# Performance work log

Measured on AMD Instinct MI355X. Metric: run time of the kernel, lower is better.

Reference implementation:

```python
import jax, jax.numpy as jnp
import numpy as np

B, NI, D, P, R = 32, 1024, 1024, 1000, 3  # batch, patches, d_model, pool_size, agg rounds


def setup_inputs() -> dict:
    key = jax.random.key(0)
    ks = jax.random.split(key, 12)
    w = lambda k, shape: jax.random.normal(k, shape, jnp.float32) * 0.02
    return {
        "att_feats": jax.random.normal(ks[0], (B, NI, D), jnp.float32),
        "fc_feats": jax.random.normal(ks[1], (B, D), jnp.float32),
        "pool": jax.random.normal(ks[2], (P, D), jnp.float32),
        "W_agg": w(ks[3], (R, D, D)),          # stacked agg projections (no bias)
        "Wq": w(ks[4], (D, D)), "bq": jnp.zeros((D,), jnp.float32),
        "Wk": w(ks[5], (D, D)), "bk": jnp.zeros((D,), jnp.float32),
        "Wv": w(ks[6], (D, D)), "bv": jnp.zeros((D,), jnp.float32),
        "Wc": w(ks[7], (D, D)), "bc": jnp.zeros((D,), jnp.float32),
        "Wg": w(ks[8], (2 * D,)), "bg": jnp.asarray(-1.0, jnp.float32),  # gate bias init -1
        "residual_scale": jnp.asarray(0.1, jnp.float32),
    }


def reference(att_feats, fc_feats, pool, W_agg, Wq, bq, Wk, bk, Wv, bv, Wc, bc, Wg, bg, residual_scale):
    d = att_feats.shape[-1]
    scale = 1.0 / jnp.sqrt(jnp.asarray(d, att_feats.dtype))
    v_hat = fc_feats  # fc dim == d_model path

    # Aggregate attention: R rounds over normality pool, averaged (Eq. 4-6)
    q_all = jnp.einsum('bd,rod->rbo', v_hat, W_agg)            # [R,B,D]
    scores = jnp.einsum('rbo,po->rbp', q_all, pool) * scale    # [R,B,P]
    weights = jax.nn.softmax(scores, axis=-1)
    v_agg = jnp.einsum('rbp,pd->bd', weights, pool) / R        # [B,D]

    # Differentiate attention (Eq. 7-10)
    q = v_hat @ Wq.T + bq
    k = v_agg @ Wk.T + bk
    v = v_agg @ Wv.T + bv
    sim = jnp.sum(q * k, axis=-1, keepdims=True) * scale       # [B,1]
    v_common = jax.nn.sigmoid(sim) * v
    v_diff = jax.nn.relu((v_hat - v_common) @ Wc.T + bc)       # [B,D] (dropout = identity, eval)

    # Gated residual; split gate weight to avoid materializing the concat
    Wg1, Wg2 = Wg[:d], Wg[d:]
    g = jax.nn.sigmoid(att_feats @ Wg1 + (v_diff @ Wg2)[:, None] + bg)  # [B,NI]
    return att_feats + residual_scale * g[..., None] * v_diff[:, None, :]
```

## Files before the change

kernel.cpp:

```cpp
#include <hip/hip_runtime.h>

#define D 1024
#define B 32
#define NI 1024
#define PP 1000
#define R 3
#define SPLITS 8
#define VS 8
#define BK 32
#define KT (D / SPLITS / BK)
#define PAD 34

typedef float f32x4_t __attribute__((ext_vector_type(4)));

__device__ __forceinline__ void nt_store4(float* p, float4 v) {
    f32x4_t x = {v.x, v.y, v.z, v.w};
    __builtin_nontemporal_store(x, (f32x4_t*)p);
}

__device__ __forceinline__ float wred(float x) {
    #pragma unroll
    for (int off = 32; off; off >>= 1) x += __shfl_xor(x, off, 64);
    return x;
}
__device__ __forceinline__ float wmax(float x) {
    #pragma unroll
    for (int off = 32; off; off >>= 1) x = fmaxf(x, __shfl_xor(x, off, 64));
    return x;
}

template<int NXS>
__device__ __forceinline__ void gemm_core(
        const float* __restrict__ A, int mbase, int Mrows,
        const float* __restrict__ Xb, int xrstride, size_t xss,
        int kc0, float acc[4][4]) {
    __shared__ float Ws[128][PAD];
    __shared__ float Xs[32][PAD];
    const int t = threadIdx.x;
    const int ty = t >> 3, tx = t & 7;
    const int m0 = 4 * ty, b0 = 4 * tx;
    const int lrow = t >> 3, lq = t & 7;

    #pragma unroll
    for (int i = 0; i < 4; ++i)
        #pragma unroll
        for (int j = 0; j < 4; ++j) acc[i][j] = 0.f;

    for (int kt = 0; kt < KT; ++kt) {
        const int kc = kc0 + kt * BK;
        #pragma unroll
        for (int rr = 0; rr < 4; ++rr) {
            const int row = lrow + 32 * rr;
            float4 v = make_float4(0.f, 0.f, 0.f, 0.f);
            if (mbase + row < Mrows)
                v = *(const float4*)(A + (size_t)(mbase + row) * D + kc + 4 * lq);
            *(float2*)&Ws[row][4 * lq]     = make_float2(v.x, v.y);
            *(float2*)&Ws[row][4 * lq + 2] = make_float2(v.z, v.w);
        }
        {
            const float* xp = Xb + (size_t)lrow * xrstride + kc + 4 * lq;
            float4 v = *(const float4*)xp;
            #pragma unroll
            for (int s = 1; s < NXS; ++s) {
                float4 w = *(const float4*)(xp + (size_t)s * xss);
                v.x += w.x; v.y += w.y; v.z += w.z; v.w += w.w;
            }
            *(float2*)&Xs[lrow][4 * lq]     = make_float2(v.x, v.y);
            *(float2*)&Xs[lrow][4 * lq + 2] = make_float2(v.z, v.w);
        }
        __syncthreads();
        #pragma unroll
        for (int kp = 0; kp < 16; ++kp) {
            float2 wv[4], xv[4];
            #pragma unroll
            for (int i = 0; i < 4; ++i) wv[i] = *(const float2*)&Ws[m0 + i][2 * kp];
            #pragma unroll
            for (int j = 0; j < 4; ++j) xv[j] = *(const float2*)&Xs[b0 + j][2 * kp];
            #pragma unroll
            for (int i = 0; i < 4; ++i)
                #pragma unroll
                for (int j = 0; j < 4; ++j) {
                    acc[i][j] += wv[i].x * xv[j].x;
                    acc[i][j] += wv[i].y * xv[j].y;
                }
        }
        __syncthreads();
    }
}

__global__ __launch_bounds__(256) void gemm_k1(const float* __restrict__ Wagg,
        const float* __restrict__ fc, float* __restrict__ Cp) {
    const int mb = blockIdx.x, s = blockIdx.y;
    const int mbase = mb * 128;
    float acc[4][4];
    gemm_core<1>(Wagg, mbase, R * D, fc, D, 0, s * 128, acc);
    const int t = threadIdx.x, ty = t >> 3, tx = t & 7;
    const int m = mbase + 4 * ty;
    #pragma unroll
    for (int j = 0; j < 4; ++j) {
        float* cp = Cp + ((size_t)(s * B) + 4 * tx + j) * (R * D) + m;
        *(float4*)cp = make_float4(acc[0][j], acc[1][j], acc[2][j], acc[3][j]);
    }
}

__global__ __launch_bounds__(256) void gemm_k2(const float* __restrict__ pool,
        const float* __restrict__ qallp, float* __restrict__ Cp) {
    const int mb = blockIdx.x, s = blockIdx.y, r = blockIdx.z;
    const int mbase = mb * 128;
    float acc[4][4];
    gemm_core<SPLITS>(pool, mbase, PP, qallp + r * D, R * D, (size_t)B * R * D,
                      s * 128, acc);
    const int t = threadIdx.x, ty = t >> 3, tx = t & 7;
    const int m = mbase + 4 * ty;
    if (m >= PP) return;
    #pragma unroll
    for (int j = 0; j < 4; ++j) {
        float* cp = Cp + ((size_t)((s * R + r) * B) + 4 * tx + j) * D + m;
        *(float4*)cp = make_float4(acc[0][j], acc[1][j], acc[2][j], acc[3][j]);
    }
}

__global__ __launch_bounds__(256) void gemm_k5q(const float* __restrict__ Wq,
        const float* __restrict__ fc, float* __restrict__ Cp) {
    const int mb = blockIdx.x, s = blockIdx.y;
    const int mbase = mb * 128;
    float acc[4][4];
    gemm_core<1>(Wq, mbase, D, fc, D, 0, s * 128, acc);
    const int t = threadIdx.x, ty = t >> 3, tx = t & 7;
    const int m = mbase + 4 * ty;
    #pragma unroll
    for (int j = 0; j < 4; ++j) {
        float* cp = Cp + ((size_t)((s * R + 0) * B) + 4 * tx + j) * D + m;
        *(float4*)cp = make_float4(acc[0][j], acc[1][j], acc[2][j], acc[3][j]);
    }
}

__global__ __launch_bounds__(256) void gemm_k5kv(const float* __restrict__ Wk,
        const float* __restrict__ Wv, const float* __restrict__ vaggp,
        float* __restrict__ Cp) {
    const int mb = blockIdx.x, s = blockIdx.y, z = blockIdx.z;
    const int mbase = mb * 128;
    const float* A = (z == 0) ? Wk : Wv;
    float acc[4][4];
    gemm_core<VS>(A, mbase, D, vaggp, D, (size_t)B * D, s * 128, acc);
    const int t = threadIdx.x, ty = t >> 3, tx = t & 7;
    const int m = mbase + 4 * ty;
    #pragma unroll
    for (int j = 0; j < 4; ++j) {
        float* cp = Cp + ((size_t)((s * R + z + 1) * B) + 4 * tx + j) * D + m;
        *(float4*)cp = make_float4(acc[0][j], acc[1][j], acc[2][j], acc[3][j]);
    }
}

__global__ __launch_bounds__(256) void gemm_k7(const float* __restrict__ Wc,
        const float* __restrict__ u, float* __restrict__ Cp) {
    const int mb = blockIdx.x, s = blockIdx.y;
    const int mbase = mb * 128;
    float acc[4][4];
    gemm_core<1>(Wc, mbase, D, u, D, 0, s * 128, acc);
    const int t = threadIdx.x, ty = t >> 3, tx = t & 7;
    const int m = mbase + 4 * ty;
    #pragma unroll
    for (int j = 0; j < 4; ++j) {
        float* cp = Cp + ((size_t)(s * B) + 4 * tx + j) * D + m;
        *(float4*)cp = make_float4(acc[0][j], acc[1][j], acc[2][j], acc[3][j]);
    }
}

__global__ __launch_bounds__(256) void k3_wbar(const float* __restrict__ scp,
        float* __restrict__ wbar) {
    const int b = blockIdx.x;
    const int t = threadIdx.x, w = t >> 6, lane = t & 63;
    __shared__ float red[8];
    float wb[4] = {0.f, 0.f, 0.f, 0.f};
    for (int r = 0; r < R; ++r) {
        float v[4];
        float mx = -1e30f;
        #pragma unroll
        for (int i = 0; i < 4; ++i) {
            const int p = t + 256 * i;
            float x = -1e30f;
            if (p < PP) {
                x = 0.f;
                #pragma unroll
                for (int s = 0; s < SPLITS; ++s)
                    x += scp[((size_t)((s * R + r) * B) + b) * D + p];
                x *= 0.03125f;
            }
            v[i] = x;
            mx = fmaxf(mx, x);
        }
        mx = wmax(mx);
        if (lane == 0) red[w] = mx;
        __syncthreads();
        mx = fmaxf(fmaxf(red[0], red[1]), fmaxf(red[2], red[3]));
        float e[4], sum = 0.f;
        #pragma unroll
        for (int i = 0; i < 4; ++i) {
            const int p = t + 256 * i;
            e[i] = (p < PP) ? __expf(v[i] - mx) : 0.f;
            sum += e[i];
        }
        sum = wred(sum);
        if (lane == 0) red[4 + w] = sum;
        __syncthreads();
        const float inv = 1.f / (red[4] + red[5] + red[6] + red[7]);
        #pragma unroll
        for (int i = 0; i < 4; ++i) wb[i] += e[i] * inv;
        __syncthreads();
    }
    #pragma unroll
    for (int i = 0; i < 4; ++i) {
        const int p = t + 256 * i;
        wbar[(size_t)b * 1024 + p] = wb[i] * (1.f / 3.f);
    }
}

__global__ __launch_bounds__(256) void k4_vagg(const float* __restrict__ wbar,
        const float* __restrict__ pool, float* __restrict__ vaggp) {
    const int db = blockIdx.x, ps = blockIdx.y;
    __shared__ float Ps[32][132];
    __shared__ float Wbt[32][36];
    const int t = threadIdx.x;
    const int ty = t >> 3, tx = t & 7;
    float acc[4][4];
    #pragma unroll
    for (int i = 0; i < 4; ++i)
        #pragma unroll
        for (int j = 0; j < 4; ++j) acc[i][j] = 0.f;

    for (int pt = 0; pt < 4; ++pt) {
        const int p0 = ps * 128 + pt * 32;
        {
            const int prow = t >> 5, qc = t & 31;
            #pragma unroll
            for (int rr = 0; rr < 4; ++rr) {
                const int pr = prow + 8 * rr;
                float4 v = make_float4(0.f, 0.f, 0.f, 0.f);
                if (p0 + pr < PP)
                    v = *(const float4*)(pool + (size_t)(p0 + pr) * D + db * 128 + 4 * qc);
                *(float4*)&Ps[pr][4 * qc] = v;
            }
        }
        {
            const int bb = t >> 3, q = t & 7;
            float4 v = *(const float4*)(wbar + (size_t)bb * 1024 + p0 + 4 * q);
            Wbt[4 * q + 0][bb] = v.x; Wbt[4 * q + 1][bb] = v.y;
            Wbt[4 * q + 2][bb] = v.z; Wbt[4 * q + 3][bb] = v.w;
        }
        __syncthreads();
        #pragma unroll
        for (int pg = 0; pg < 8; ++pg) {
            #pragma unroll
            for (int pp = 0; pp < 4; ++pp) {
                const int p = 4 * pg + pp;
                float4 xv = *(const float4*)&Ps[p][4 * ty];
                float4 wv = *(const float4*)&Wbt[p][4 * tx];
                const float xs[4] = {xv.x, xv.y, xv.z, xv.w};
                const float wsv[4] = {wv.x, wv.y, wv.z, wv.w};
                #pragma unroll
                for (int i = 0; i < 4; ++i)
                    #pragma unroll
                    for (int j = 0; j < 4; ++j)
                        acc[i][j] += xs[i] * wsv[j];
            }
        }
        __syncthreads();
    }
    const int dbase = db * 128 + 4 * ty;
    #pragma unroll
    for (int j = 0; j < 4; ++j) {
        float* op = vaggp + ((size_t)ps * B + 4 * tx + j) * D + dbase;
        *(float4*)op = make_float4(acc[0][j], acc[1][j], acc[2][j], acc[3][j]);
    }
}

__global__ __launch_bounds__(256) void k6_u(const float* __restrict__ qkvp,
        const float* __restrict__ bq, const float* __restrict__ bk,
        const float* __restrict__ bv, const float* __restrict__ vhat,
        float* __restrict__ u) {
    const int b = blockIdx.x;
    const int t = threadIdx.x, w = t >> 6, lane = t & 63;
    const int d = 4 * t;
    float4 qv = *(const float4*)(bq + d);
    float4 kv = *(const float4*)(bk + d);
    #pragma unroll
    for (int s = 0; s < SPLITS; ++s) {
        float4 a = *(const float4*)(qkvp + ((size_t)((s * R + 0) * B) + b) * D + d);
        float4 c = *(const float4*)(qkvp + ((size_t)((s * R + 1) * B) + b) * D + d);
        qv.x += a.x; qv.y += a.y; qv.z += a.z; qv.w += a.w;
        kv.x += c.x; kv.y += c.y; kv.z += c.z; kv.w += c.w;
    }
    float local = qv.x * kv.x + qv.y * kv.y + qv.z * kv.z + qv.w * kv.w;
    local = wred(local);
    __shared__ float red[4];
    if (lane == 0) red[w] = local;
    __syncthreads();
    const float sim = (red[0] + red[1] + red[2] + red[3]) * 0.03125f;
    const float sig = 1.f / (1.f + __expf(-sim));
    float4 vv = *(const float4*)(bv + d);
    #pragma unroll
    for (int s = 0; s < SPLITS; ++s) {
        float4 c = *(const float4*)(qkvp + ((size_t)((s * R + 2) * B) + b) * D + d);
        vv.x += c.x; vv.y += c.y; vv.z += c.z; vv.w += c.w;
    }
    const float4 vh = *(const float4*)(vhat + (size_t)b * D + d);
    float4 o;
    o.x = vh.x - sig * vv.x; o.y = vh.y - sig * vv.y;
    o.z = vh.z - sig * vv.z; o.w = vh.w - sig * vv.w;
    *(float4*)(u + (size_t)b * D + d) = o;
}

__global__ __launch_bounds__(256) void k8_cb(const float* __restrict__ vdp,
        const float* __restrict__ bc, const float* __restrict__ Wg,
        const float* __restrict__ bg, float* __restrict__ vdiff,
        float* __restrict__ cb) {
    const int b = blockIdx.x;
    const int t = threadIdx.x, w = t >> 6, lane = t & 63;
    const int d = 4 * t;
    float4 a = *(const float4*)(bc + d);
    #pragma unroll
    for (int s = 0; s < SPLITS; ++s) {
        float4 c = *(const float4*)(vdp + ((size_t)(s * B) + b) * D + d);
        a.x += c.x; a.y += c.y; a.z += c.z; a.w += c.w;
    }
    a.x = fmaxf(a.x, 0.f); a.y = fmaxf(a.y, 0.f);
    a.z = fmaxf(a.z, 0.f); a.w = fmaxf(a.w, 0.f);
    *(float4*)(vdiff + (size_t)b * D + d) = a;
    const float4 g2 = *(const float4*)(Wg + D + d);
    float local = a.x * g2.x + a.y * g2.y + a.z * g2.z + a.w * g2.w;
    local = wred(local);
    __shared__ float red[4];
    if (lane == 0) red[w] = local;
    __syncthreads();
    if (t == 0) cb[b] = red[0] + red[1] + red[2] + red[3] + bg[0];
}

__global__ __launch_bounds__(256) void k9_main(const float* __restrict__ att,
        const float* __restrict__ Wg, const float* __restrict__ cb,
        const float* __restrict__ vdiff, const float* __restrict__ rs_p,
        float* __restrict__ out) {
    __shared__ float wgs[1024];
    __shared__ float vds[1024];
    const int t = threadIdx.x;
    const int b = blockIdx.x >> 6;
    *(float4*)&wgs[4 * t] = *(const float4*)(Wg + 4 * t);
    *(float4*)&vds[4 * t] = *(const float4*)(vdiff + (size_t)b * D + 4 * t);
    __syncthreads();
    const int w = t >> 6, lane = t & 63;
    const float rsv = rs_p[0];
    const float cbb = cb[b];
    const size_t row0 = (size_t)blockIdx.x * 16 + w * 4;

    float4 a[4][4];
    #pragma unroll
    for (int rr = 0; rr < 4; ++rr) {
        const float* arow = att + (row0 + rr) * D;
        #pragma unroll
        for (int kk = 0; kk < 4; ++kk)
            a[rr][kk] = *(const float4*)(arow + 4 * lane + 256 * kk);
    }
    float acc[4];
    #pragma unroll
    for (int rr = 0; rr < 4; ++rr) {
        float s = 0.f;
        #pragma unroll
        for (int kk = 0; kk < 4; ++kk) {
            const int col = 4 * lane + 256 * kk;
            float4 g = *(const float4*)&wgs[col];
            s += a[rr][kk].x * g.x + a[rr][kk].y * g.y +
                 a[rr][kk].z * g.z + a[rr][kk].w * g.w;
        }
        acc[rr] = s;
    }
    #pragma unroll
    for (int off = 32; off; off >>= 1) {
        #pragma unroll
        for (int rr = 0; rr < 4; ++rr) acc[rr] += __shfl_xor(acc[rr], off, 64);
    }
    #pragma unroll
    for (int rr = 0; rr < 4; ++rr) {
        const float gv = 1.f / (1.f + __expf(-(acc[rr] + cbb)));
        const float grs = gv * rsv;
        float* orow = out + (row0 + rr) * D;
        #pragma unroll
        for (int kk = 0; kk < 4; ++kk) {
            const int col = 4 * lane + 256 * kk;
            float4 vd = *(const float4*)&vds[col];
            float4 o;
            o.x = a[rr][kk].x + grs * vd.x; o.y = a[rr][kk].y + grs * vd.y;
            o.z = a[rr][kk].z + grs * vd.z; o.w = a[rr][kk].w + grs * vd.w;
            nt_store4(orow + col, o);
        }
    }
}

extern "C" void kernel_launch(void* const* d_in, const int* in_sizes, int n_in,
                              void* d_out, int out_size, void* d_ws, size_t ws_size,
                              hipStream_t stream) {
    const float* att  = (const float*)d_in[0];
    const float* fc   = (const float*)d_in[1];
    const float* pool = (const float*)d_in[2];
    const float* Wagg = (const float*)d_in[3];
    const float* Wq   = (const float*)d_in[4];
    const float* bq   = (const float*)d_in[5];
    const float* Wk   = (const float*)d_in[6];
    const float* bk   = (const float*)d_in[7];
    const float* Wv   = (const float*)d_in[8];
    const float* bv   = (const float*)d_in[9];
    const float* Wc   = (const float*)d_in[10];
    const float* bc   = (const float*)d_in[11];
    const float* Wg   = (const float*)d_in[12];
    const float* bg   = (const float*)d_in[13];
    const float* rs   = (const float*)d_in[14];
    float* out = (float*)d_out;

    float* ws = (float*)d_ws;
    float* qallp = ws;
    float* scp   = qallp + (size_t)SPLITS * B * R * D;
    float* wbar  = scp + (size_t)SPLITS * R * B * D;
    float* vaggp = wbar + (size_t)B * 1024;
    float* qkvp  = vaggp + (size_t)VS * B * D;
    float* ub    = qkvp + (size_t)SPLITS * R * B * D;
    float* vdp   = ub + (size_t)B * D;
    float* vdiff = vdp + (size_t)SPLITS * B * D;
    float* cbuf  = vdiff + (size_t)B * D;

    gemm_k1<<<dim3(24, SPLITS), 256, 0, stream>>>(Wagg, fc, qallp);
    gemm_k5q<<<dim3(8, SPLITS), 256, 0, stream>>>(Wq, fc, qkvp);
    gemm_k2<<<dim3(8, SPLITS, R), 256, 0, stream>>>(pool, qallp, scp);
    k3_wbar<<<B, 256, 0, stream>>>(scp, wbar);
    k4_vagg<<<dim3(8, VS), 256, 0, stream>>>(wbar, pool, vaggp);
    gemm_k5kv<<<dim3(8, SPLITS, 2), 256, 0, stream>>>(Wk, Wv, vaggp, qkvp);
    k6_u<<<B, 256, 0, stream>>>(qkvp, bq, bk, bv, fc, ub);
    gemm_k7<<<dim3(8, SPLITS), 256, 0, stream>>>(Wc, ub, vdp);
    k8_cb<<<B, 256, 0, stream>>>(vdp, bc, Wg, bg, vdiff, cbuf);
    k9_main<<<B * NI / 16, 256, 0, stream>>>(att, Wg, cbuf, vdiff, rs, out);
}
```

Baseline: 143.3 us.

## Split gated residual into early gate-dot pass and later apply pass

Moves the att·Wg1 row dot products into a separate kernel launched first, before the small projection GEMM chain. A second kernel then computes the sigmoid gate and writes the residual output. The apparent aim is to take the dot-product reduction off the critical tail. In exchange, att is streamed from memory twice, and everything runs on one stream, so the two passes cannot overlap.

```diff
diff --git a/kernel.cpp b/kernel.cpp
--- a/kernel.cpp
+++ b/kernel.cpp
@@ -336,62 +336,59 @@
     if (t == 0) cb[b] = red[0] + red[1] + red[2] + red[3] + bg[0];
 }
 
-__global__ __launch_bounds__(256) void k9_main(const float* __restrict__ att,
-        const float* __restrict__ Wg, const float* __restrict__ cb,
+__global__ __launch_bounds__(256) void k9a_dotg(const float* __restrict__ att,
+        const float* __restrict__ Wg, float* __restrict__ dotg) {
+    __shared__ float wgs[1024];
+    const int t = threadIdx.x;
+    *(float4*)&wgs[4 * t] = *(const float4*)(Wg + 4 * t);
+    __syncthreads();
+    const int w = t >> 6, lane = t & 63;
+    const size_t row0 = (size_t)blockIdx.x * 16 + w * 4;
+    float acc[4] = {0.f, 0.f, 0.f, 0.f};
+    #pragma unroll
+    for (int kk = 0; kk < 4; ++kk) {
+        const int col = 4 * lane + 256 * kk;
+        const float4 g = *(const float4*)&wgs[col];
+        #pragma unroll
+        for (int rr = 0; rr < 4; ++rr) {
+            float4 a = *(const float4*)(att + (row0 + rr) * D + col);
+            acc[rr] += a.x * g.x + a.y * g.y + a.z * g.z + a.w * g.w;
+        }
+    }
+    #pragma unroll
+    for (int off = 32; off; off >>= 1) {
+        #pragma unroll
+        for (int rr = 0; rr < 4; ++rr) acc[rr] += __shfl_xor(acc[rr], off, 64);
+    }
+    if (lane == 0) {
+        dotg[row0 + 0] = acc[0];
+        dotg[row0 + 1] = acc[1];
+        dotg[row0 + 2] = acc[2];
+        dotg[row0 + 3] = acc[3];
+    }
+}
+
+__global__ __launch_bounds__(256) void k9b_apply(const float* __restrict__ att,
+        const float* __restrict__ dotg, const float* __restrict__ cb,
         const float* __restrict__ vdiff, const float* __restrict__ rs_p,
         float* __restrict__ out) {
-    __shared__ float wgs[1024];
-    __shared__ float vds[1024];
     const int t = threadIdx.x;
-    const int b = blockIdx.x >> 6;
-    *(float4*)&wgs[4 * t] = *(const float4*)(Wg + 4 * t);
-    *(float4*)&vds[4 * t] = *(const float4*)(vdiff + (size_t)b * D + 4 * t);
-    __syncthreads();
-    const int w = t >> 6, lane = t & 63;
-    const float rsv = rs_p[0];
-    const float cbb = cb[b];
-    const size_t row0 = (size_t)blockIdx.x * 16 + w * 4;
-
-    float4 a[4][4];
-    #pragma unroll
-    for (int rr = 0; rr < 4; ++rr) {
-        const float* arow = att + (row0 + rr) * D;
-        #pragma unroll
-        for (int kk = 0; kk < 4; ++kk)
-            a[rr][kk] = *(const float4*)(arow + 4 * lane + 256 * kk);
-    }
-    float acc[4];
-    #pragma unroll
-    for (int rr = 0; rr < 4; ++rr) {
-        float s = 0.f;
-        #pragma unroll
-        for (int kk = 0; kk < 4; ++kk) {
-            const int col = 4 * lane + 256 * kk;
-            float4 g = *(const float4*)&wgs[col];
-            s += a[rr][kk].x * g.x + a[rr][kk].y * g.y +
-                 a[rr][kk].z * g.z + a[rr][kk].w * g.w;
-        }
-        acc[rr] = s;
-    }
-    #pragma unroll
-    for (int off = 32; off; off >>= 1) {
-        #pragma unroll
-        for (int rr = 0; rr < 4; ++rr) acc[rr] += __shfl_xor(acc[rr], off, 64);
-    }
-    #pragma unroll
-    for (int rr = 0; rr < 4; ++rr) {
-        const float gv = 1.f / (1.f + __expf(-(acc[rr] + cbb)));
-        const float grs = gv * rsv;
-        float* orow = out + (row0 + rr) * D;
-        #pragma unroll
-        for (int kk = 0; kk < 4; ++kk) {
-            const int col = 4 * lane + 256 * kk;
-            float4 vd = *(const float4*)&vds[col];
-            float4 o;
-            o.x = a[rr][kk].x + grs * vd.x; o.y = a[rr][kk].y + grs * vd.y;
-            o.z = a[rr][kk].z + grs * vd.z; o.w = a[rr][kk].w + grs * vd.w;
-            nt_store4(orow + col, o);
-        }
+    const int r = t >> 6, lane = t & 63;
+    const size_t row = (size_t)blockIdx.x * 4 + r;
+    const int b = (int)(row >> 10);
+    const float grs = rs_p[0] / (1.f + __expf(-(dotg[row] + cb[b])));
+    const float* arow = att + row * D;
+    const float* vrow = vdiff + (size_t)b * D;
+    float* orow = out + row * D;
+    #pragma unroll
+    for (int kk = 0; kk < 4; ++kk) {
+        const int col = (kk * 64 + lane) * 4;
+        float4 a = *(const float4*)(arow + col);
+        float4 vd = *(const float4*)(vrow + col);
+        float4 o;
+        o.x = a.x + grs * vd.x; o.y = a.y + grs * vd.y;
+        o.z = a.z + grs * vd.z; o.w = a.w + grs * vd.w;
+        nt_store4(orow + col, o);
     }
 }
 
@@ -425,6 +422,9 @@
     float* vdp   = ub + (size_t)B * D;
     float* vdiff = vdp + (size_t)SPLITS * B * D;
     float* cbuf  = vdiff + (size_t)B * D;
+    float* dotg  = cbuf + 64;
+
+    k9a_dotg<<<B * NI / 16, 256, 0, stream>>>(att, Wg, dotg);
 
     gemm_k1<<<dim3(24, SPLITS), 256, 0, stream>>>(Wagg, fc, qallp);
     gemm_k5q<<<dim3(8, SPLITS), 256, 0, stream>>>(Wq, fc, qkvp);
@@ -435,5 +435,6 @@
     k6_u<<<B, 256, 0, stream>>>(qkvp, bq, bk, bv, fc, ub);
     gemm_k7<<<dim3(8, SPLITS), 256, 0, stream>>>(Wc, ub, vdp);
     k8_cb<<<B, 256, 0, stream>>>(vdp, bc, Wg, bg, vdiff, cbuf);
-    k9_main<<<B * NI / 16, 256, 0, stream>>>(att, Wg, cbuf, vdiff, rs, out);
-}
+
+    k9b_apply<<<B * NI / 4, 256, 0, stream>>>(att, dotg, cbuf, vdiff, rs, out);
+}
```

Measured after the change: 164.9 us. 15.0% more time.

## Merge Q/K/V projection launches and software-pipeline the gated residual kernel

Applied to the files above, without the earlier changes.

The separate Wq projection launch is folded into the K/V projection kernel as a third z-slice, which removes one kernel launch from the chain. The main streaming kernel now handles 32 rows per block, eight per wave, two rows at a time. It prefetches the next pair of att rows into registers while the current pair is reduced and stored, and keeps the Wg vector in registers instead of shared memory. This aims to hide memory latency on the bandwidth-bound 128MB read plus write, at the cost of higher register pressure, fewer blocks, and branch divergence across the merged GEMM slices.

```diff
diff --git a/kernel.cpp b/kernel.cpp
--- a/kernel.cpp
+++ b/kernel.cpp
@@ -120,34 +120,23 @@
     }
 }
 
-__global__ __launch_bounds__(256) void gemm_k5q(const float* __restrict__ Wq,
-        const float* __restrict__ fc, float* __restrict__ Cp) {
-    const int mb = blockIdx.x, s = blockIdx.y;
-    const int mbase = mb * 128;
-    float acc[4][4];
-    gemm_core<1>(Wq, mbase, D, fc, D, 0, s * 128, acc);
-    const int t = threadIdx.x, ty = t >> 3, tx = t & 7;
-    const int m = mbase + 4 * ty;
-    #pragma unroll
-    for (int j = 0; j < 4; ++j) {
-        float* cp = Cp + ((size_t)((s * R + 0) * B) + 4 * tx + j) * D + m;
-        *(float4*)cp = make_float4(acc[0][j], acc[1][j], acc[2][j], acc[3][j]);
-    }
-}
-
-__global__ __launch_bounds__(256) void gemm_k5kv(const float* __restrict__ Wk,
-        const float* __restrict__ Wv, const float* __restrict__ vaggp,
+__global__ __launch_bounds__(256) void gemm_k5(const float* __restrict__ Wq,
+        const float* __restrict__ Wk, const float* __restrict__ Wv,
+        const float* __restrict__ fc, const float* __restrict__ vaggp,
         float* __restrict__ Cp) {
     const int mb = blockIdx.x, s = blockIdx.y, z = blockIdx.z;
     const int mbase = mb * 128;
-    const float* A = (z == 0) ? Wk : Wv;
     float acc[4][4];
-    gemm_core<VS>(A, mbase, D, vaggp, D, (size_t)B * D, s * 128, acc);
+    if (z == 0)
+        gemm_core<1>(Wq, mbase, D, fc, D, 0, s * 128, acc);
+    else
+        gemm_core<VS>((z == 1) ? Wk : Wv, mbase, D, vaggp, D, (size_t)B * D,
+                      s * 128, acc);
     const int t = threadIdx.x, ty = t >> 3, tx = t & 7;
     const int m = mbase + 4 * ty;
     #pragma unroll
     for (int j = 0; j < 4; ++j) {
-        float* cp = Cp + ((size_t)((s * R + z + 1) * B) + 4 * tx + j) * D + m;
+        float* cp = Cp + ((size_t)((s * R + z) * B) + 4 * tx + j) * D + m;
         *(float4*)cp = make_float4(acc[0][j], acc[1][j], acc[2][j], acc[3][j]);
     }
 }
@@ -336,61 +325,70 @@
     if (t == 0) cb[b] = red[0] + red[1] + red[2] + red[3] + bg[0];
 }
 
-__global__ __launch_bounds__(256) void k9_main(const float* __restrict__ att,
+__global__ __launch_bounds__(256, 4) void k9_main(const float* __restrict__ att,
         const float* __restrict__ Wg, const float* __restrict__ cb,
         const float* __restrict__ vdiff, const float* __restrict__ rs_p,
         float* __restrict__ out) {
-    __shared__ float wgs[1024];
     __shared__ float vds[1024];
     const int t = threadIdx.x;
-    const int b = blockIdx.x >> 6;
-    *(float4*)&wgs[4 * t] = *(const float4*)(Wg + 4 * t);
+    const int b = blockIdx.x >> 5;
     *(float4*)&vds[4 * t] = *(const float4*)(vdiff + (size_t)b * D + 4 * t);
     __syncthreads();
     const int w = t >> 6, lane = t & 63;
+    float4 g[4];
+    #pragma unroll
+    for (int kk = 0; kk < 4; ++kk)
+        g[kk] = *(const float4*)(Wg + 4 * lane + 256 * kk);
     const float rsv = rs_p[0];
     const float cbb = cb[b];
-    const size_t row0 = (size_t)blockIdx.x * 16 + w * 4;
-
-    float4 a[4][4];
-    #pragma unroll
-    for (int rr = 0; rr < 4; ++rr) {
-        const float* arow = att + (row0 + rr) * D;
-        #pragma unroll
-        for (int kk = 0; kk < 4; ++kk)
-            a[rr][kk] = *(const float4*)(arow + 4 * lane + 256 * kk);
-    }
-    float acc[4];
-    #pragma unroll
-    for (int rr = 0; rr < 4; ++rr) {
-        float s = 0.f;
+    const size_t row0 = (size_t)b * NI + (size_t)(blockIdx.x & 31) * 32 + w * 8;
+    const float* ap = att + row0 * D;
+    float* op = out + row0 * D;
+
+    float4 cur[8], nxt[8];
+    #pragma unroll
+    for (int q = 0; q < 8; ++q)
+        cur[q] = *(const float4*)(ap + (size_t)(q >> 2) * D + 4 * lane + 256 * (q & 3));
+
+    #pragma unroll
+    for (int it = 0; it < 4; ++it) {
+        if (it < 3) {
+            const float* apn = ap + (size_t)(2 * it + 2) * D;
+            #pragma unroll
+            for (int q = 0; q < 8; ++q)
+                nxt[q] = *(const float4*)(apn + (size_t)(q >> 2) * D + 4 * lane + 256 * (q & 3));
+        }
+        float acc0 = 0.f, acc1 = 0.f;
+        #pragma unroll
+        for (int kk = 0; kk < 4; ++kk) {
+            acc0 += cur[kk].x * g[kk].x + cur[kk].y * g[kk].y +
+                    cur[kk].z * g[kk].z + cur[kk].w * g[kk].w;
+            acc1 += cur[4 + kk].x * g[kk].x + cur[4 + kk].y * g[kk].y +
+                    cur[4 + kk].z * g[kk].z + cur[4 + kk].w * g[kk].w;
+        }
+        #pragma unroll
+        for (int off = 32; off; off >>= 1) {
+            acc0 += __shfl_xor(acc0, off, 64);
+            acc1 += __shfl_xor(acc1, off, 64);
+        }
+        const float grs0 = rsv / (1.f + __expf(-(acc0 + cbb)));
+        const float grs1 = rsv / (1.f + __expf(-(acc1 + cbb)));
+        float* op0 = op + (size_t)(2 * it) * D;
         #pragma unroll
         for (int kk = 0; kk < 4; ++kk) {
             const int col = 4 * lane + 256 * kk;
-            float4 g = *(const float4*)&wgs[col];
-            s += a[rr][kk].x * g.x + a[rr][kk].y * g.y +
-                 a[rr][kk].z * g.z + a[rr][kk].w * g.w;
-        }
-        acc[rr] = s;
-    }
-    #pragma unroll
-    for (int off = 32; off; off >>= 1) {
-        #pragma unroll
-        for (int rr = 0; rr < 4; ++rr) acc[rr] += __shfl_xor(acc[rr], off, 64);
-    }
-    #pragma unroll
-    for (int rr = 0; rr < 4; ++rr) {
-        const float gv = 1.f / (1.f + __expf(-(acc[rr] + cbb)));
-        const float grs = gv * rsv;
-        float* orow = out + (row0 + rr) * D;
-        #pragma unroll
-        for (int kk = 0; kk < 4; ++kk) {
-            const int col = 4 * lane + 256 * kk;
-            float4 vd = *(const float4*)&vds[col];
-            float4 o;
-            o.x = a[rr][kk].x + grs * vd.x; o.y = a[rr][kk].y + grs * vd.y;
-            o.z = a[rr][kk].z + grs * vd.z; o.w = a[rr][kk].w + grs * vd.w;
-            nt_store4(orow + col, o);
+            const float4 vd = *(const float4*)&vds[col];
+            float4 o0, o1;
+            o0.x = cur[kk].x + grs0 * vd.x; o0.y = cur[kk].y + grs0 * vd.y;
+            o0.z = cur[kk].z + grs0 * vd.z; o0.w = cur[kk].w + grs0 * vd.w;
+            o1.x = cur[4 + kk].x + grs1 * vd.x; o1.y = cur[4 + kk].y + grs1 * vd.y;
+            o1.z = cur[4 + kk].z + grs1 * vd.z; o1.w = cur[4 + kk].w + grs1 * vd.w;
+            nt_store4(op0 + col, o0);
+            nt_store4(op0 + D + col, o1);
+        }
+        if (it < 3) {
+            #pragma unroll
+            for (int q = 0; q < 8; ++q) cur[q] = nxt[q];
         }
     }
 }
@@ -427,13 +425,12 @@
     float* cbuf  = vdiff + (size_t)B * D;
 
     gemm_k1<<<dim3(24, SPLITS), 256, 0, stream>>>(Wagg, fc, qallp);
-    gemm_k5q<<<dim3(8, SPLITS), 256, 0, stream>>>(Wq, fc, qkvp);
     gemm_k2<<<dim3(8, SPLITS, R), 256, 0, stream>>>(pool, qallp, scp);
     k3_wbar<<<B, 256, 0, stream>>>(scp, wbar);
     k4_vagg<<<dim3(8, VS), 256, 0, stream>>>(wbar, pool, vaggp);
-    gemm_k5kv<<<dim3(8, SPLITS, 2), 256, 0, stream>>>(Wk, Wv, vaggp, qkvp);
+    gemm_k5<<<dim3(8, SPLITS, R), 256, 0, stream>>>(Wq, Wk, Wv, fc, vaggp, qkvp);
     k6_u<<<B, 256, 0, stream>>>(qkvp, bq, bk, bv, fc, ub);
     gemm_k7<<<dim3(8, SPLITS), 256, 0, stream>>>(Wc, ub, vdp);
     k8_cb<<<B, 256, 0, stream>>>(vdp, bc, Wg, bg, vdiff, cbuf);
-    k9_main<<<B * NI / 16, 256, 0, stream>>>(att, Wg, cbuf, vdiff, rs, out);
-}
+    k9_main<<<B * 32, 256, 0, stream>>>(att, Wg, cbuf, vdiff, rs, out);
+}
```

Measured after the change: 130.5 us. 1.1x faster.
